# Kernel optimization log

Measured on AMD Instinct MI355X. Metric: run time of the kernel, lower is better.

The kernel has to match this reference:

```python
import jax, jax.numpy as jnp
import numpy as np

B, N, F = 512, 64, 64
ROBOT_DIM, HUMAN_DIM, HID = 9, 5, 128
K = 3  # Chebyshev order


def setup_inputs() -> dict:
    key = jax.random.key(0)
    ks = jax.random.split(key, 16)
    # complete directed graph without self loops, shared across the batch
    src, dst = np.nonzero(~np.eye(N, dtype=bool))
    edge_index = jnp.asarray(np.stack([src, dst]), dtype=jnp.int32)  # [2, E]
    s = 0.05
    return {
        "robot_x": jax.random.normal(ks[0], (B, 1, ROBOT_DIM), jnp.float32),
        "human_x": jax.random.normal(ks[1], (B, N - 1, HUMAN_DIM), jnp.float32),
        "edge_index": edge_index,
        "wr1_w": jax.random.normal(ks[2], (ROBOT_DIM, HID), jnp.float32) * s,
        "wr1_b": jax.random.normal(ks[3], (HID,), jnp.float32) * s,
        "wr2_w": jax.random.normal(ks[4], (HID, F), jnp.float32) * s,
        "wr2_b": jax.random.normal(ks[5], (F,), jnp.float32) * s,
        "wh1_w": jax.random.normal(ks[6], (HUMAN_DIM, HID), jnp.float32) * s,
        "wh1_b": jax.random.normal(ks[7], (HID,), jnp.float32) * s,
        "wh2_w": jax.random.normal(ks[8], (HID, F), jnp.float32) * s,
        "wh2_b": jax.random.normal(ks[9], (F,), jnp.float32) * s,
        "cheb_w": jax.random.normal(ks[10], (K, F, F), jnp.float32) * s,
        "cheb_b": jax.random.normal(ks[11], (F,), jnp.float32) * s,
    }


def reference(robot_x, human_x, edge_index, wr1_w, wr1_b, wr2_w, wr2_b,
              wh1_w, wh1_b, wh2_w, wh2_b, cheb_w, cheb_b):
    # MLP embeddings with last_relu=True
    r = jax.nn.relu(robot_x @ wr1_w + wr1_b)
    r = jax.nn.relu(r @ wr2_w + wr2_b)            # [B, 1, F]
    h = jax.nn.relu(human_x @ wh1_w + wh1_b)
    h = jax.nn.relu(h @ wh2_w + wh2_b)            # [B, N-1, F]
    X = jnp.concatenate([r, h], axis=1)           # [B, N, F]

    src, dst = edge_index[0], edge_index[1]
    n = X.shape[1]
    # PyG ChebConv sym-normalized scaled Laplacian with lambda_max=2:
    # L_hat = -D^{-1/2} A D^{-1/2}  (edge weights all ones, no self loops)
    deg = jax.ops.segment_sum(jnp.ones(src.shape[0], X.dtype), src, num_segments=n)
    dinv = jnp.where(deg > 0, deg ** -0.5, 0.0)
    w = -(dinv[src] * dinv[dst])                  # [E]

    def prop(x):  # x: [B, N, F] -> L_hat @ x per batch via gather/scatter
        msg = x[:, src, :] * w[None, :, None]     # [B, E, F]
        return jnp.zeros_like(x).at[:, dst, :].add(msg)

    Tx0 = X
    Tx1 = prop(X)
    Tx2 = 2.0 * prop(Tx1) - Tx0
    Tx = jnp.stack([Tx0, Tx1, Tx2], axis=0)       # [K, B, N, F]
    out = jnp.einsum("kbnf,kfo->bno", Tx, cheb_w) + cheb_b
    return out[:, 0, :]                           # robot node output [B, F]
```

## Files before the change

kernel.cpp:

```cpp
#include <hip/hip_runtime.h>


#define BDIM 512

typedef __attribute__((ext_vector_type(8))) short bf16x8;
typedef __attribute__((ext_vector_type(4))) float f32x4;

static __device__ __forceinline__ unsigned short f2bf(float f) {
    unsigned int u = __float_as_uint(f);
    u += 0x7FFF + ((u >> 16) & 1);
    return (unsigned short)(u >> 16);
}

__global__ __launch_bounds__(512, 4) void dgcrnn_mfma(
    const float* __restrict__ robot_x,
    const float* __restrict__ human_x,
    const float* __restrict__ wr1, const float* __restrict__ wr1_b,
    const float* __restrict__ wr2, const float* __restrict__ wr2_b,
    const float* __restrict__ wh1, const float* __restrict__ wh1_b,
    const float* __restrict__ wh2, const float* __restrict__ wh2_b,
    const float* __restrict__ cw,  const float* __restrict__ cb,
    float* __restrict__ out)
{
    __shared__ float x_lds[324];
    __shared__ float wh1_l[768];
    __shared__ float wr1_l[1280];
    __shared__ float wh2b_l[64];
    __shared__ float rrow[128];
    __shared__ __align__(16) unsigned int wh2T[4096];
    __shared__ __align__(16) short fragA[8192];
    __shared__ __align__(16) float rp_lds[2048];
    __shared__ float hpart[256];
    __shared__ float r_s[64], s_s[64];

    const int t   = threadIdx.x;
    const int b   = blockIdx.x;
    const int l   = t & 63;
    const int w   = t >> 6;
    const int oq  = t & 15;
    const int o0  = oq * 4;
    const int g16 = t >> 4;

    float4 wr2q[4];
    #pragma unroll
    for (int j = 0; j < 4; ++j)
        wr2q[j] = *(const float4*)&wr2[(g16 * 4 + j) * 64 + o0];
    float4 cwq[2][3];
    #pragma unroll
    for (int ff = 0; ff < 2; ++ff)
        #pragma unroll
        for (int k = 0; k < 3; ++k)
            cwq[ff][k] = *(const float4*)&cw[k * 4096 + (g16 * 2 + ff) * 64 + o0];

    for (int i = t; i < 324; i += BDIM)
        x_lds[i] = (i < 9) ? robot_x[b * 9 + i] : human_x[b * 315 + (i - 9)];
    for (int i = t; i < 768; i += BDIM)
        wh1_l[i] = (i < 640) ? wh1[i] : wh1_b[i - 640];
    for (int i = t; i < 1280; i += BDIM)
        wr1_l[i] = (i < 1152) ? wr1[i] : wr1_b[i - 1152];
    if (t < 64) wh2b_l[t] = wh2_b[t];
    #pragma unroll
    for (int kk = 0; kk < 2; ++kk) {
        int kp = g16 * 2 + kk;
        float4 e = *(const float4*)&wh2[(2 * kp) * 64 + o0];
        float4 d = *(const float4*)&wh2[(2 * kp + 1) * 64 + o0];
        #pragma unroll
        for (int c = 0; c < 4; ++c) {
            int o = o0 + c;
            unsigned int wv = (unsigned int)f2bf((&e.x)[c])
                            | ((unsigned int)f2bf((&d.x)[c]) << 16);
            wh2T[o * 64 + (kp ^ ((o & 15) << 2))] = wv;
        }
    }
    __syncthreads();

    #pragma unroll
    for (int s = 0; s < 2; ++s) {
        int slot = s * 512 + t;
        int row  = ((slot >> 8) << 4) | (slot & 15);
        int k0   = ((slot >> 6) & 3) * 32 + ((slot >> 4) & 3) * 8;
        bf16x8 v;
        #pragma unroll
        for (int j = 0; j < 8; ++j) v[j] = 0;
        if (row != 63) {
            float a8[8];
            #pragma unroll
            for (int j = 0; j < 8; ++j) a8[j] = wh1_l[640 + k0 + j];
            #pragma unroll
            for (int i = 0; i < 5; ++i) {
                float xv = x_lds[9 + row * 5 + i];
                #pragma unroll
                for (int j = 0; j < 8; ++j)
                    a8[j] = fmaf(xv, wh1_l[i * 128 + k0 + j], a8[j]);
            }
            #pragma unroll
            for (int j = 0; j < 8; ++j) v[j] = (short)f2bf(fmaxf(a8[j], 0.f));
        }
        *reinterpret_cast<bf16x8*>(&fragA[slot * 8]) = v;
    }
    if (t < 128) {
        float a = wr1_l[1152 + t];
        #pragma unroll
        for (int i = 0; i < 9; ++i) a = fmaf(x_lds[i], wr1_l[i * 128 + t], a);
        rrow[t] = fmaxf(a, 0.f);
    }
    __syncthreads();

    {
        float4 rp = {0.f, 0.f, 0.f, 0.f};
        #pragma unroll
        for (int j = 0; j < 4; ++j) {
            float hv = rrow[g16 * 4 + j];
            rp.x = fmaf(hv, wr2q[j].x, rp.x);
            rp.y = fmaf(hv, wr2q[j].y, rp.y);
            rp.z = fmaf(hv, wr2q[j].z, rp.z);
            rp.w = fmaf(hv, wr2q[j].w, rp.w);
        }
        *(float4*)&rp_lds[g16 * 64 + o0] = rp;
    }

    {
        const int c = l & 15, g = l >> 4;
        const int mt = w >> 1;
        bf16x8 af[4];
        #pragma unroll
        for (int kt = 0; kt < 4; ++kt)
            af[kt] = *reinterpret_cast<const bf16x8*>(&fragA[((mt * 4 + kt) * 64 + l) * 8]);
        #pragma unroll
        for (int ni = 0; ni < 2; ++ni) {
            const int nt = (w & 1) * 2 + ni;
            const int o  = nt * 16 + c;
            f32x4 acc = {0.f, 0.f, 0.f, 0.f};
            #pragma unroll
            for (int kt = 0; kt < 4; ++kt) {
                int kw0 = kt * 16 + g * 4;
                bf16x8 bfv = *reinterpret_cast<const bf16x8*>(
                    &wh2T[o * 64 + (kw0 ^ (c << 2))]);
                acc = __builtin_amdgcn_mfma_f32_16x16x32_bf16(af[kt], bfv, acc, 0, 0, 0);
            }
            float bias = wh2b_l[o];
            float s4 = 0.f;
            #pragma unroll
            for (int reg = 0; reg < 4; ++reg) {
                int node = mt * 16 + g * 4 + reg;
                float hv = fmaxf(acc[reg] + bias, 0.f);
                s4 += (node == 63) ? 0.f : hv;
            }
            s4 += __shfl_xor(s4, 16, 64);
            s4 += __shfl_xor(s4, 32, 64);
            if (g == 0) hpart[mt * 64 + o] = s4;
        }
    }
    __syncthreads();

    if (t < 64) {
        float hs = hpart[t] + hpart[64 + t] + hpart[128 + t] + hpart[192 + t];
        float rsum = wr2_b[t];
        #pragma unroll
        for (int kg = 0; kg < 32; ++kg) rsum += rp_lds[kg * 64 + t];
        float r = fmaxf(rsum, 0.f);
        r_s[t] = r;
        s_s[t] = r + hs;
    }
    __syncthreads();

    {
        const float c1 = 1.0f / 63.0f;
        const float c2 = 2.0f / 3969.0f - 1.0f;
        const float c3 = 124.0f / 3969.0f;
        float4 a4 = {0.f, 0.f, 0.f, 0.f};
        #pragma unroll
        for (int ff = 0; ff < 2; ++ff) {
            int f = g16 * 2 + ff;
            float rv = r_s[f], sv = s_s[f];
            #pragma unroll
            for (int c = 0; c < 4; ++c) {
                float w0  = (&cwq[ff][0].x)[c];
                float w1  = (&cwq[ff][1].x)[c];
                float w2v = (&cwq[ff][2].x)[c];
                (&a4.x)[c] += rv * (w0 + c1 * w1 + c2 * w2v)
                            + sv * (c3 * w2v - c1 * w1);
            }
        }
        *(float4*)&rp_lds[g16 * 64 + o0] = a4;
    }
    __syncthreads();
    if (t < 64) {
        float a = cb[t];
        #pragma unroll
        for (int kg = 0; kg < 32; ++kg) a += rp_lds[kg * 64 + t];
        out[b * 64 + t] = a;
    }
}

extern "C" void kernel_launch(void* const* d_in, const int* in_sizes, int n_in,
                              void* d_out, int out_size, void* d_ws, size_t ws_size,
                              hipStream_t stream) {
    const float* robot_x = (const float*)d_in[0];
    const float* human_x = (const float*)d_in[1];
    const float* wr1   = (const float*)d_in[3];
    const float* wr1_b = (const float*)d_in[4];
    const float* wr2   = (const float*)d_in[5];
    const float* wr2_b = (const float*)d_in[6];
    const float* wh1   = (const float*)d_in[7];
    const float* wh1_b = (const float*)d_in[8];
    const float* wh2   = (const float*)d_in[9];
    const float* wh2_b = (const float*)d_in[10];
    const float* cw    = (const float*)d_in[11];
    const float* cb    = (const float*)d_in[12];
    float* out = (float*)d_out;

    dgcrnn_mfma<<<512, BDIM, 0, stream>>>(robot_x, human_x,
                                          wr1, wr1_b, wr2, wr2_b,
                                          wh1, wh1_b, wh2, wh2_b,
                                          cw, cb, out);
}
```

Measured before the change: 12.42 us.

## Halve block size to 256 threads and remove a barrier stage

The block shrinks from 512 to 256 threads, so each thread handles twice the work: four fragA slots, four MFMA N-tiles per wave, and eight wr2 rows. The r/s reduction is folded into the final Chebyshev combine, which removes one __syncthreads and the r_s/s_s staging. wr1 weights now sit in registers instead of LDS, and biases are preloaded into LDS. The aim is less barrier and LDS overhead per block, at the cost of more registers per thread and redundant reductions, since every thread recomputes rsum for its four features.

```diff
diff --git a/kernel.cpp b/kernel.cpp
--- a/kernel.cpp
+++ b/kernel.cpp
@@ -1,7 +1,7 @@
 #include <hip/hip_runtime.h>
 
 
-#define BDIM 512
+#define BDIM 256
 
 typedef __attribute__((ext_vector_type(8))) short bf16x8;
 typedef __attribute__((ext_vector_type(4))) float f32x4;
@@ -12,7 +12,7 @@
     return (unsigned short)(u >> 16);
 }
 
-__global__ __launch_bounds__(512, 4) void dgcrnn_mfma(
+__global__ __launch_bounds__(256, 2) void dgcrnn_mfma(
     const float* __restrict__ robot_x,
     const float* __restrict__ human_x,
     const float* __restrict__ wr1, const float* __restrict__ wr1_b,
@@ -24,44 +24,40 @@
 {
     __shared__ float x_lds[324];
     __shared__ float wh1_l[768];
-    __shared__ float wr1_l[1280];
-    __shared__ float wh2b_l[64];
+    __shared__ float wh2b_l[64], wr2b_l[64], cb_l[64];
     __shared__ float rrow[128];
     __shared__ __align__(16) unsigned int wh2T[4096];
     __shared__ __align__(16) short fragA[8192];
-    __shared__ __align__(16) float rp_lds[2048];
+    __shared__ __align__(16) float rp_lds[1024];
     __shared__ float hpart[256];
-    __shared__ float r_s[64], s_s[64];
-
-    const int t   = threadIdx.x;
-    const int b   = blockIdx.x;
-    const int l   = t & 63;
-    const int w   = t >> 6;
-    const int oq  = t & 15;
-    const int o0  = oq * 4;
-    const int g16 = t >> 4;
-
-    float4 wr2q[4];
+
+    const int t    = threadIdx.x;
+    const int b    = blockIdx.x;
+    const int l    = t & 63;
+    const int w    = t >> 6;
+    const int oq   = t & 15;
+    const int o0   = oq * 4;
+    const int fgrp = t >> 4;
+
+    float4 wr2q[8];
     #pragma unroll
-    for (int j = 0; j < 4; ++j)
-        wr2q[j] = *(const float4*)&wr2[(g16 * 4 + j) * 64 + o0];
-    float4 cwq[2][3];
-    #pragma unroll
-    for (int ff = 0; ff < 2; ++ff)
-        #pragma unroll
-        for (int k = 0; k < 3; ++k)
-            cwq[ff][k] = *(const float4*)&cw[k * 4096 + (g16 * 2 + ff) * 64 + o0];
+    for (int j = 0; j < 8; ++j)
+        wr2q[j] = *(const float4*)&wr2[(fgrp * 8 + j) * 64 + o0];
+    float wr1c[9], wr1bb = 0.f;
+    if (t < 128) {
+        #pragma unroll
+        for (int i = 0; i < 9; ++i) wr1c[i] = wr1[i * 128 + t];
+        wr1bb = wr1_b[t];
+    }
 
     for (int i = t; i < 324; i += BDIM)
         x_lds[i] = (i < 9) ? robot_x[b * 9 + i] : human_x[b * 315 + (i - 9)];
     for (int i = t; i < 768; i += BDIM)
         wh1_l[i] = (i < 640) ? wh1[i] : wh1_b[i - 640];
-    for (int i = t; i < 1280; i += BDIM)
-        wr1_l[i] = (i < 1152) ? wr1[i] : wr1_b[i - 1152];
-    if (t < 64) wh2b_l[t] = wh2_b[t];
+    if (t < 64) { wh2b_l[t] = wh2_b[t]; wr2b_l[t] = wr2_b[t]; cb_l[t] = cb[t]; }
     #pragma unroll
-    for (int kk = 0; kk < 2; ++kk) {
-        int kp = g16 * 2 + kk;
+    for (int kk = 0; kk < 4; ++kk) {
+        int kp = fgrp * 4 + kk;
         float4 e = *(const float4*)&wh2[(2 * kp) * 64 + o0];
         float4 d = *(const float4*)&wh2[(2 * kp + 1) * 64 + o0];
         #pragma unroll
@@ -74,62 +70,55 @@
     }
     __syncthreads();
 
-    #pragma unroll
-    for (int s = 0; s < 2; ++s) {
-        int slot = s * 512 + t;
-        int row  = ((slot >> 8) << 4) | (slot & 15);
-        int k0   = ((slot >> 6) & 3) * 32 + ((slot >> 4) & 3) * 8;
-        bf16x8 v;
-        #pragma unroll
-        for (int j = 0; j < 8; ++j) v[j] = 0;
-        if (row != 63) {
-            float a8[8];
-            #pragma unroll
-            for (int j = 0; j < 8; ++j) a8[j] = wh1_l[640 + k0 + j];
-            #pragma unroll
-            for (int i = 0; i < 5; ++i) {
-                float xv = x_lds[9 + row * 5 + i];
+    {
+        const int k0 = ((t >> 6) & 3) * 32 + ((t >> 4) & 3) * 8;
+        float wv[5][8], bias8[8];
+        #pragma unroll
+        for (int j = 0; j < 8; ++j) bias8[j] = wh1_l[640 + k0 + j];
+        #pragma unroll
+        for (int i = 0; i < 5; ++i)
+            #pragma unroll
+            for (int j = 0; j < 8; ++j) wv[i][j] = wh1_l[i * 128 + k0 + j];
+        #pragma unroll
+        for (int s = 0; s < 4; ++s) {
+            int slot = s * 256 + t;
+            int row  = (s << 4) | (t & 15);
+            bf16x8 v;
+            #pragma unroll
+            for (int j = 0; j < 8; ++j) v[j] = 0;
+            if (row != 63) {
+                float a8[8];
                 #pragma unroll
-                for (int j = 0; j < 8; ++j)
-                    a8[j] = fmaf(xv, wh1_l[i * 128 + k0 + j], a8[j]);
-            }
-            #pragma unroll
-            for (int j = 0; j < 8; ++j) v[j] = (short)f2bf(fmaxf(a8[j], 0.f));
-        }
-        *reinterpret_cast<bf16x8*>(&fragA[slot * 8]) = v;
+                for (int j = 0; j < 8; ++j) a8[j] = bias8[j];
+                #pragma unroll
+                for (int i = 0; i < 5; ++i) {
+                    float xv = x_lds[9 + row * 5 + i];
+                    #pragma unroll
+                    for (int j = 0; j < 8; ++j) a8[j] = fmaf(xv, wv[i][j], a8[j]);
+                }
+                #pragma unroll
+                for (int j = 0; j < 8; ++j) v[j] = (short)f2bf(fmaxf(a8[j], 0.f));
+            }
+            *reinterpret_cast<bf16x8*>(&fragA[slot * 8]) = v;
+        }
     }
     if (t < 128) {
-        float a = wr1_l[1152 + t];
-        #pragma unroll
-        for (int i = 0; i < 9; ++i) a = fmaf(x_lds[i], wr1_l[i * 128 + t], a);
+        float a = wr1bb;
+        #pragma unroll
+        for (int i = 0; i < 9; ++i) a = fmaf(x_lds[i], wr1c[i], a);
         rrow[t] = fmaxf(a, 0.f);
     }
     __syncthreads();
 
     {
-        float4 rp = {0.f, 0.f, 0.f, 0.f};
-        #pragma unroll
-        for (int j = 0; j < 4; ++j) {
-            float hv = rrow[g16 * 4 + j];
-            rp.x = fmaf(hv, wr2q[j].x, rp.x);
-            rp.y = fmaf(hv, wr2q[j].y, rp.y);
-            rp.z = fmaf(hv, wr2q[j].z, rp.z);
-            rp.w = fmaf(hv, wr2q[j].w, rp.w);
-        }
-        *(float4*)&rp_lds[g16 * 64 + o0] = rp;
-    }
-
-    {
-        const int c = l & 15, g = l >> 4;
-        const int mt = w >> 1;
+        const int c = l & 15, g = l >> 4, mt = w;
         bf16x8 af[4];
         #pragma unroll
         for (int kt = 0; kt < 4; ++kt)
             af[kt] = *reinterpret_cast<const bf16x8*>(&fragA[((mt * 4 + kt) * 64 + l) * 8]);
         #pragma unroll
-        for (int ni = 0; ni < 2; ++ni) {
-            const int nt = (w & 1) * 2 + ni;
-            const int o  = nt * 16 + c;
+        for (int nt = 0; nt < 4; ++nt) {
+            const int o = nt * 16 + c;
             f32x4 acc = {0.f, 0.f, 0.f, 0.f};
             #pragma unroll
             for (int kt = 0; kt < 4; ++kt) {
@@ -151,17 +140,26 @@
             if (g == 0) hpart[mt * 64 + o] = s4;
         }
     }
-    __syncthreads();
-
-    if (t < 64) {
-        float hs = hpart[t] + hpart[64 + t] + hpart[128 + t] + hpart[192 + t];
-        float rsum = wr2_b[t];
-        #pragma unroll
-        for (int kg = 0; kg < 32; ++kg) rsum += rp_lds[kg * 64 + t];
-        float r = fmaxf(rsum, 0.f);
-        r_s[t] = r;
-        s_s[t] = r + hs;
-    }
+
+    {
+        float4 rp = {0.f, 0.f, 0.f, 0.f};
+        #pragma unroll
+        for (int j = 0; j < 8; ++j) {
+            float hv = rrow[fgrp * 8 + j];
+            rp.x = fmaf(hv, wr2q[j].x, rp.x);
+            rp.y = fmaf(hv, wr2q[j].y, rp.y);
+            rp.z = fmaf(hv, wr2q[j].z, rp.z);
+            rp.w = fmaf(hv, wr2q[j].w, rp.w);
+        }
+        *(float4*)&rp_lds[fgrp * 64 + o0] = rp;
+    }
+
+    float4 cwq[4][3];
+    #pragma unroll
+    for (int ff = 0; ff < 4; ++ff)
+        #pragma unroll
+        for (int k = 0; k < 3; ++k)
+            cwq[ff][k] = *(const float4*)&cw[k * 4096 + (fgrp * 4 + ff) * 64 + o0];
     __syncthreads();
 
     {
@@ -170,9 +168,13 @@
         const float c3 = 124.0f / 3969.0f;
         float4 a4 = {0.f, 0.f, 0.f, 0.f};
         #pragma unroll
-        for (int ff = 0; ff < 2; ++ff) {
-            int f = g16 * 2 + ff;
-            float rv = r_s[f], sv = s_s[f];
+        for (int ff = 0; ff < 4; ++ff) {
+            int f = fgrp * 4 + ff;
+            float rsum = wr2b_l[f];
+            #pragma unroll
+            for (int kg = 0; kg < 16; ++kg) rsum += rp_lds[kg * 64 + f];
+            float rv = fmaxf(rsum, 0.f);
+            float sv = rv + hpart[f] + hpart[64 + f] + hpart[128 + f] + hpart[192 + f];
             #pragma unroll
             for (int c = 0; c < 4; ++c) {
                 float w0  = (&cwq[ff][0].x)[c];
@@ -182,13 +184,16 @@
                             + sv * (c3 * w2v - c1 * w1);
             }
         }
-        *(float4*)&rp_lds[g16 * 64 + o0] = a4;
-    }
-    __syncthreads();
+        float* out_part = reinterpret_cast<float*>(fragA);
+        *(float4*)&out_part[fgrp * 64 + o0] = a4;
+    }
+    __syncthreads();
+
     if (t < 64) {
-        float a = cb[t];
-        #pragma unroll
-        for (int kg = 0; kg < 32; ++kg) a += rp_lds[kg * 64 + t];
+        const float* out_part = reinterpret_cast<const float*>(fragA);
+        float a = cb_l[t];
+        #pragma unroll
+        for (int kg = 0; kg < 16; ++kg) a += out_part[kg * 64 + t];
         out[b * 64 + t] = a;
     }
 }
```

New measurement: 11.97 us. -3.6%, faster.
